# Optimization experiments

Measured on AMD Instinct MI355X. Metric: run time of the kernel, lower is better.

Reference implementation:

```python
import jax, jax.numpy as jnp
import numpy as np

B, N, F = 64, 512, 128

def setup_inputs() -> dict:
    key = jax.random.key(0)
    k1, k2 = jax.random.split(key)
    inp = jax.random.normal(k1, (B, N, F), dtype=jnp.float32)
    valid_mask = jnp.ones((B, N, N), dtype=jnp.float32)
    weight = 0.1 * jax.random.normal(k2, (N, N), dtype=jnp.float32)
    return {"input": inp, "valid_mask": valid_mask, "weight": weight}

def reference(input, valid_mask, weight):
    # softmax over last dim of weight, broadcast over batch
    adj = jax.nn.softmax(weight, axis=-1)[None, :, :] * valid_mask  # [B,N,N]
    n = weight.shape[0]
    adj = adj + jnp.eye(n, dtype=adj.dtype)[None, :, :]
    # symmetric degree normalization D^-1/2 A D^-1/2 (D diagonal of row sums).
    # Original builds dense D and does two matmuls; diagonal scaling is the
    # identical math expressed as row/col broadcast.
    row_sum = adj.sum(axis=2)  # [B,N]
    d = jnp.where(row_sum > 0, jax.lax.rsqrt(row_sum), 0.0)  # inf -> 0 handling
    adj_nor = d[:, :, None] * adj * d[:, None, :]  # [B,N,N]
    return jnp.matmul(adj_nor, input)  # [B,N,F]
```

## Files before the change

kernel.cpp:

```cpp
#include <hip/hip_runtime.h>
#include <math.h>

#define BB 64
#define NN 512
#define FF 128

typedef __bf16 bf16x8 __attribute__((ext_vector_type(8)));
typedef float floatx4 __attribute__((ext_vector_type(4)));

__device__ __forceinline__ unsigned int bf16u(float f) {
    unsigned int u = __builtin_bit_cast(unsigned int, f);
    unsigned int r = (u + 0x7FFFu + ((u >> 16) & 1u)) >> 16;
    return r & 0xFFFFu;
}

__global__ __launch_bounds__(256) void softmax_kernel(const float* __restrict__ w,
                                                      float* __restrict__ S) {
    const int row = blockIdx.x;
    const float* wr = w + (size_t)row * NN;
    float* sr = S + (size_t)row * NN;
    const int tid = threadIdx.x;
    const int wave = tid >> 6, lane = tid & 63;

    float v0 = wr[tid];
    float v1 = wr[tid + 256];

    float m = fmaxf(v0, v1);
    #pragma unroll
    for (int off = 32; off > 0; off >>= 1)
        m = fmaxf(m, __shfl_down(m, off, 64));
    __shared__ float red[8];
    if (lane == 0) red[wave] = m;
    __syncthreads();
    if (tid == 0) red[4] = fmaxf(fmaxf(red[0], red[1]), fmaxf(red[2], red[3]));
    __syncthreads();
    m = red[4];

    float e0 = expf(v0 - m);
    float e1 = expf(v1 - m);

    float s = e0 + e1;
    #pragma unroll
    for (int off = 32; off > 0; off >>= 1)
        s += __shfl_down(s, off, 64);
    __syncthreads();
    if (lane == 0) red[wave] = s;
    __syncthreads();
    if (tid == 0) red[5] = 1.0f / (red[0] + red[1] + red[2] + red[3]);
    __syncthreads();
    const float inv = red[5];

    sr[tid]       = e0 * inv;
    sr[tid + 256] = e1 * inv;
}

__global__ __launch_bounds__(256) void rowsum_kernel(const float* __restrict__ S,
                                                     const float* __restrict__ mask,
                                                     float* __restrict__ dvec) {
    const int b = blockIdx.x >> 5;
    const int g = blockIdx.x & 31;
    const int r = threadIdx.x >> 4;
    const int l = threadIdx.x & 15;
    const int i = g * 16 + r;

    const float4* mrow = (const float4*)(mask + ((size_t)b * NN + i) * NN);
    const float4* srow = (const float4*)(S + (size_t)i * NN);

    float sum = 0.f;
    #pragma unroll
    for (int k = 0; k < 8; ++k) {
        float4 mv = mrow[l + 16 * k];
        float4 sv = srow[l + 16 * k];
        sum += mv.x * sv.x + mv.y * sv.y + mv.z * sv.z + mv.w * sv.w;
    }
    #pragma unroll
    for (int off = 8; off > 0; off >>= 1)
        sum += __shfl_down(sum, off, 16);
    if (l == 0) {
        float rs = sum + 1.0f;
        dvec[b * NN + i] = (rs > 0.f) ? (1.0f / sqrtf(rs)) : 0.f;
    }
}

#define PADT 129
__global__ __launch_bounds__(256) void xt_kernel(const float* __restrict__ in,
                                                 const float* __restrict__ dvec,
                                                 unsigned short* __restrict__ Xt) {
    __shared__ unsigned short T[64 * PADT];
    const int b = blockIdx.y;
    const int j0 = blockIdx.x * 64;
    const int tid = threadIdx.x;

    const int fg = tid & 31;
    const int jr = tid >> 5;
    #pragma unroll
    for (int p = 0; p < 8; ++p) {
        int j = jr + 8 * p;
        float dj = dvec[b * NN + j0 + j];
        float4 xv = *(const float4*)(in + ((size_t)b * NN + j0 + j) * FF + 4 * fg);
        T[j * PADT + 4 * fg + 0] = (unsigned short)bf16u(xv.x * dj);
        T[j * PADT + 4 * fg + 1] = (unsigned short)bf16u(xv.y * dj);
        T[j * PADT + 4 * fg + 2] = (unsigned short)bf16u(xv.z * dj);
        T[j * PADT + 4 * fg + 3] = (unsigned short)bf16u(xv.w * dj);
    }
    __syncthreads();

    const int c = tid & 7;
    const int fr = tid >> 3;
    #pragma unroll
    for (int q = 0; q < 4; ++q) {
        int f = fr + 32 * q;
        unsigned int v01 = (unsigned int)T[(8 * c + 0) * PADT + f] |
                           ((unsigned int)T[(8 * c + 1) * PADT + f] << 16);
        unsigned int v23 = (unsigned int)T[(8 * c + 2) * PADT + f] |
                           ((unsigned int)T[(8 * c + 3) * PADT + f] << 16);
        unsigned int v45 = (unsigned int)T[(8 * c + 4) * PADT + f] |
                           ((unsigned int)T[(8 * c + 5) * PADT + f] << 16);
        unsigned int v67 = (unsigned int)T[(8 * c + 6) * PADT + f] |
                           ((unsigned int)T[(8 * c + 7) * PADT + f] << 16);
        uint4 pk = make_uint4(v01, v23, v45, v67);
        *(uint4*)(Xt + ((size_t)b * FF + f) * NN + j0 + 8 * c) = pk;
    }
}

#define TI 32
#define ASTR 72
__global__ __launch_bounds__(256) void matmul_kernel(const float* __restrict__ S,
                                                     const float* __restrict__ mask,
                                                     const float* __restrict__ dvec,
                                                     const unsigned short* __restrict__ Xt,
                                                     const float* __restrict__ in,
                                                     float* __restrict__ out) {
    __shared__ __align__(16) unsigned short Alds[2][TI * ASTR];

    const int b = blockIdx.y;
    const int i_base = blockIdx.x * TI;
    const int tid = threadIdx.x;
    const int w = tid >> 6;
    const int lane = tid & 63;
    const int quad = lane >> 4;
    const int l16 = lane & 15;
    const int iw = (w & 1) * 16;
    const int fw = (w >> 1) * 64;

    const float* dB = dvec + b * NN;
    const unsigned short* XtB = Xt + (size_t)b * FF * NN;

    floatx4 acc[4];
    #pragma unroll
    for (int nt = 0; nt < 4; nt++) acc[nt] = (floatx4){0.f, 0.f, 0.f, 0.f};

    const int a_il = tid >> 3;
    const int a_js = (tid & 7) * 8;
    const float* mbase = mask + ((size_t)b * NN + i_base + a_il) * NN + a_js;
    const float* sbase = S + (size_t)(i_base + a_il) * NN + a_js;
    unsigned short* awr = &Alds[0][0] + a_il * ASTR + a_js;

    {
        float4 m0 = *(const float4*)(mbase);
        float4 m1 = *(const float4*)(mbase + 4);
        float4 s0 = *(const float4*)(sbase);
        float4 s1 = *(const float4*)(sbase + 4);
        uint4 pk;
        pk.x = bf16u(m0.x * s0.x) | (bf16u(m0.y * s0.y) << 16);
        pk.y = bf16u(m0.z * s0.z) | (bf16u(m0.w * s0.w) << 16);
        pk.z = bf16u(m1.x * s1.x) | (bf16u(m1.y * s1.y) << 16);
        pk.w = bf16u(m1.z * s1.z) | (bf16u(m1.w * s1.w) << 16);
        *(uint4*)awr = pk;
    }

    #pragma unroll
    for (int c = 0; c < 8; ++c) {
        const int p = c & 1;
        float4 m0, m1, s0, s1;
        if (c < 7) {
            int jn = (c + 1) * 64;
            m0 = *(const float4*)(mbase + jn);
            m1 = *(const float4*)(mbase + jn + 4);
            s0 = *(const float4*)(sbase + jn);
            s1 = *(const float4*)(sbase + jn + 4);
        }
        __syncthreads();

        const int j0 = c * 64;
        bf16x8 bfr[2][4];
        #pragma unroll
        for (int s = 0; s < 2; ++s)
            #pragma unroll
            for (int nt = 0; nt < 4; ++nt)
                bfr[s][nt] = *(const bf16x8*)&XtB[(size_t)(fw + nt * 16 + l16) * NN + j0 + s * 32 + quad * 8];
        #pragma unroll
        for (int s = 0; s < 2; ++s) {
            bf16x8 af = *(const bf16x8*)&Alds[p][(iw + l16) * ASTR + s * 32 + quad * 8];
            #pragma unroll
            for (int nt = 0; nt < 4; ++nt)
                acc[nt] = __builtin_amdgcn_mfma_f32_16x16x32_bf16(af, bfr[s][nt], acc[nt], 0, 0, 0);
        }

        if (c < 7) {
            uint4 pk;
            pk.x = bf16u(m0.x * s0.x) | (bf16u(m0.y * s0.y) << 16);
            pk.y = bf16u(m0.z * s0.z) | (bf16u(m0.w * s0.w) << 16);
            pk.z = bf16u(m1.x * s1.x) | (bf16u(m1.y * s1.y) << 16);
            pk.w = bf16u(m1.z * s1.z) | (bf16u(m1.w * s1.w) << 16);
            *(uint4*)(&Alds[p ^ 1][0] + a_il * ASTR + a_js) = pk;
        }
    }

    #pragma unroll
    for (int nt = 0; nt < 4; nt++) {
        int f = fw + nt * 16 + l16;
        #pragma unroll
        for (int r = 0; r < 4; r++) {
            int i = i_base + iw + quad * 4 + r;
            float di = dB[i];
            float x = in[((size_t)b * NN + i) * FF + f];
            out[((size_t)b * NN + i) * FF + f] = di * (acc[nt][r] + di * x);
        }
    }
}

extern "C" void kernel_launch(void* const* d_in, const int* in_sizes, int n_in,
                              void* d_out, int out_size, void* d_ws, size_t ws_size,
                              hipStream_t stream) {
    const float* inp  = (const float*)d_in[0];
    const float* mask = (const float*)d_in[1];
    const float* w    = (const float*)d_in[2];
    float* out = (float*)d_out;

    unsigned short* Xt = (unsigned short*)d_ws;
    float* S    = (float*)(Xt + (size_t)BB * FF * NN);
    float* dvec = S + (size_t)NN * NN;

    softmax_kernel<<<NN, 256, 0, stream>>>(w, S);
    rowsum_kernel<<<BB * 32, 256, 0, stream>>>(S, mask, dvec);
    dim3 gx(NN / 64, BB);
    xt_kernel<<<gx, 256, 0, stream>>>(inp, dvec, Xt);
    dim3 g3(NN / TI, BB);
    matmul_kernel<<<g3, 256, 0, stream>>>(S, mask, dvec, Xt, inp, out);
}
```

Baseline: 154.2 us.

## Fuse softmax with rowsum, shrink matmul row tile, prefetch B fragments

Merges the softmax and the masked row-sum/rsqrt into one kernel. Each block recomputes the softmax row and handles 16 batches for that row, which removes one launch and the global reread of S for the row sums. The matmul tile shrinks from 32 to 16 rows, doubling the block count to 2048 for better occupancy. Each wave now covers 32 features, so X fragments are reloaded by more blocks and reuse drops. The Xt fragments are also register-prefetched one chunk ahead to hide global load latency.

```diff
diff --git a/kernel.cpp b/kernel.cpp
--- a/kernel.cpp
+++ b/kernel.cpp
@@ -4,6 +4,9 @@
 #define BB 64
 #define NN 512
 #define FF 128
+#define ASTR 72
+#define PADT 129
+#define TI2 16
 
 typedef __bf16 bf16x8 __attribute__((ext_vector_type(8)));
 typedef float floatx4 __attribute__((ext_vector_type(4)));
@@ -14,23 +17,24 @@
     return r & 0xFFFFu;
 }
 
-__global__ __launch_bounds__(256) void softmax_kernel(const float* __restrict__ w,
-                                                      float* __restrict__ S) {
+__global__ __launch_bounds__(256) void softmax_rowsum_kernel(
+        const float* __restrict__ w, const float* __restrict__ mask,
+        float* __restrict__ S, float* __restrict__ dvec) {
+    __shared__ float Srow[NN];
+    __shared__ float red[8];
     const int row = blockIdx.x;
-    const float* wr = w + (size_t)row * NN;
-    float* sr = S + (size_t)row * NN;
+    const int bg = blockIdx.y;
     const int tid = threadIdx.x;
-    const int wave = tid >> 6, lane = tid & 63;
-
-    float v0 = wr[tid];
-    float v1 = wr[tid + 256];
+    const int wv = tid >> 6, lane = tid & 63;
+
+    float v0 = w[(size_t)row * NN + tid];
+    float v1 = w[(size_t)row * NN + tid + 256];
 
     float m = fmaxf(v0, v1);
     #pragma unroll
     for (int off = 32; off > 0; off >>= 1)
         m = fmaxf(m, __shfl_down(m, off, 64));
-    __shared__ float red[8];
-    if (lane == 0) red[wave] = m;
+    if (lane == 0) red[wv] = m;
     __syncthreads();
     if (tid == 0) red[4] = fmaxf(fmaxf(red[0], red[1]), fmaxf(red[2], red[3]));
     __syncthreads();
@@ -38,51 +42,52 @@
 
     float e0 = expf(v0 - m);
     float e1 = expf(v1 - m);
-
     float s = e0 + e1;
     #pragma unroll
     for (int off = 32; off > 0; off >>= 1)
         s += __shfl_down(s, off, 64);
     __syncthreads();
-    if (lane == 0) red[wave] = s;
+    if (lane == 0) red[wv] = s;
     __syncthreads();
     if (tid == 0) red[5] = 1.0f / (red[0] + red[1] + red[2] + red[3]);
     __syncthreads();
     const float inv = red[5];
-
-    sr[tid]       = e0 * inv;
-    sr[tid + 256] = e1 * inv;
-}
-
-__global__ __launch_bounds__(256) void rowsum_kernel(const float* __restrict__ S,
-                                                     const float* __restrict__ mask,
-                                                     float* __restrict__ dvec) {
-    const int b = blockIdx.x >> 5;
-    const int g = blockIdx.x & 31;
-    const int r = threadIdx.x >> 4;
-    const int l = threadIdx.x & 15;
-    const int i = g * 16 + r;
-
-    const float4* mrow = (const float4*)(mask + ((size_t)b * NN + i) * NN);
-    const float4* srow = (const float4*)(S + (size_t)i * NN);
-
-    float sum = 0.f;
-    #pragma unroll
-    for (int k = 0; k < 8; ++k) {
-        float4 mv = mrow[l + 16 * k];
-        float4 sv = srow[l + 16 * k];
-        sum += mv.x * sv.x + mv.y * sv.y + mv.z * sv.z + mv.w * sv.w;
-    }
-    #pragma unroll
-    for (int off = 8; off > 0; off >>= 1)
-        sum += __shfl_down(sum, off, 16);
-    if (l == 0) {
-        float rs = sum + 1.0f;
-        dvec[b * NN + i] = (rs > 0.f) ? (1.0f / sqrtf(rs)) : 0.f;
-    }
-}
-
-#define PADT 129
+    const float s0v = e0 * inv, s1v = e1 * inv;
+
+    Srow[tid] = s0v;
+    Srow[tid + 256] = s1v;
+    if (bg == 0) {
+        S[(size_t)row * NN + tid] = s0v;
+        S[(size_t)row * NN + tid + 256] = s1v;
+    }
+    __syncthreads();
+
+    float4 sA = *(const float4*)&Srow[lane * 8];
+    float4 sB = *(const float4*)&Srow[lane * 8 + 4];
+
+    float4 mA[4], mB[4];
+    #pragma unroll
+    for (int t = 0; t < 4; ++t) {
+        int b = bg * 16 + wv * 4 + t;
+        const float4* mrow = (const float4*)(mask + ((size_t)b * NN + row) * NN);
+        mA[t] = mrow[2 * lane];
+        mB[t] = mrow[2 * lane + 1];
+    }
+    #pragma unroll
+    for (int t = 0; t < 4; ++t) {
+        float sum = mA[t].x * sA.x + mA[t].y * sA.y + mA[t].z * sA.z + mA[t].w * sA.w
+                  + mB[t].x * sB.x + mB[t].y * sB.y + mB[t].z * sB.z + mB[t].w * sB.w;
+        #pragma unroll
+        for (int off = 32; off > 0; off >>= 1)
+            sum += __shfl_down(sum, off, 64);
+        if (lane == 0) {
+            int b = bg * 16 + wv * 4 + t;
+            float rs = sum + 1.0f;
+            dvec[b * NN + row] = (rs > 0.f) ? (1.0f / sqrtf(rs)) : 0.f;
+        }
+    }
+}
+
 __global__ __launch_bounds__(256) void xt_kernel(const float* __restrict__ in,
                                                  const float* __restrict__ dvec,
                                                  unsigned short* __restrict__ Xt) {
@@ -104,7 +109,6 @@
         T[j * PADT + 4 * fg + 3] = (unsigned short)bf16u(xv.w * dj);
     }
     __syncthreads();
-
     const int c = tid & 7;
     const int fr = tid >> 3;
     #pragma unroll
@@ -118,101 +122,96 @@
                            ((unsigned int)T[(8 * c + 5) * PADT + f] << 16);
         unsigned int v67 = (unsigned int)T[(8 * c + 6) * PADT + f] |
                            ((unsigned int)T[(8 * c + 7) * PADT + f] << 16);
-        uint4 pk = make_uint4(v01, v23, v45, v67);
-        *(uint4*)(Xt + ((size_t)b * FF + f) * NN + j0 + 8 * c) = pk;
-    }
-}
-
-#define TI 32
-#define ASTR 72
-__global__ __launch_bounds__(256) void matmul_kernel(const float* __restrict__ S,
-                                                     const float* __restrict__ mask,
-                                                     const float* __restrict__ dvec,
-                                                     const unsigned short* __restrict__ Xt,
-                                                     const float* __restrict__ in,
-                                                     float* __restrict__ out) {
-    __shared__ __align__(16) unsigned short Alds[2][TI * ASTR];
+        *(uint4*)(Xt + ((size_t)b * FF + f) * NN + j0 + 8 * c) = make_uint4(v01, v23, v45, v67);
+    }
+}
+
+__global__ __launch_bounds__(256) void matmul_kernel(
+        const float* __restrict__ S, const float* __restrict__ mask,
+        const float* __restrict__ dvec, const unsigned short* __restrict__ Xt,
+        const float* __restrict__ in, float* __restrict__ out) {
+    __shared__ __align__(16) unsigned short Alds[2][TI2 * ASTR];
 
     const int b = blockIdx.y;
-    const int i_base = blockIdx.x * TI;
+    const int i_base = blockIdx.x * TI2;
     const int tid = threadIdx.x;
-    const int w = tid >> 6;
+    const int wv = tid >> 6;
     const int lane = tid & 63;
     const int quad = lane >> 4;
     const int l16 = lane & 15;
-    const int iw = (w & 1) * 16;
-    const int fw = (w >> 1) * 64;
+    const int fw = wv * 32;
 
     const float* dB = dvec + b * NN;
     const unsigned short* XtB = Xt + (size_t)b * FF * NN;
 
-    floatx4 acc[4];
-    #pragma unroll
-    for (int nt = 0; nt < 4; nt++) acc[nt] = (floatx4){0.f, 0.f, 0.f, 0.f};
-
-    const int a_il = tid >> 3;
-    const int a_js = (tid & 7) * 8;
+    floatx4 acc[2];
+    acc[0] = (floatx4){0.f, 0.f, 0.f, 0.f};
+    acc[1] = (floatx4){0.f, 0.f, 0.f, 0.f};
+
+    const int a_il = tid >> 4;
+    const int a_js = (tid & 15) * 4;
     const float* mbase = mask + ((size_t)b * NN + i_base + a_il) * NN + a_js;
     const float* sbase = S + (size_t)(i_base + a_il) * NN + a_js;
-    unsigned short* awr = &Alds[0][0] + a_il * ASTR + a_js;
 
     {
-        float4 m0 = *(const float4*)(mbase);
-        float4 m1 = *(const float4*)(mbase + 4);
-        float4 s0 = *(const float4*)(sbase);
-        float4 s1 = *(const float4*)(sbase + 4);
-        uint4 pk;
+        float4 m0 = *(const float4*)mbase;
+        float4 s0 = *(const float4*)sbase;
+        uint2 pk;
         pk.x = bf16u(m0.x * s0.x) | (bf16u(m0.y * s0.y) << 16);
         pk.y = bf16u(m0.z * s0.z) | (bf16u(m0.w * s0.w) << 16);
-        pk.z = bf16u(m1.x * s1.x) | (bf16u(m1.y * s1.y) << 16);
-        pk.w = bf16u(m1.z * s1.z) | (bf16u(m1.w * s1.w) << 16);
-        *(uint4*)awr = pk;
-    }
+        *(uint2*)(&Alds[0][0] + a_il * ASTR + a_js) = pk;
+    }
+    bf16x8 bcur[4];
+    #pragma unroll
+    for (int s = 0; s < 2; ++s)
+        #pragma unroll
+        for (int nt = 0; nt < 2; ++nt)
+            bcur[s * 2 + nt] = *(const bf16x8*)&XtB[(size_t)(fw + nt * 16 + l16) * NN + s * 32 + quad * 8];
 
     #pragma unroll
     for (int c = 0; c < 8; ++c) {
         const int p = c & 1;
-        float4 m0, m1, s0, s1;
+        float4 m0, s0;
+        if (c < 7) {
+            m0 = *(const float4*)(mbase + (c + 1) * 64);
+            s0 = *(const float4*)(sbase + (c + 1) * 64);
+        }
+        __syncthreads();
+
+        bf16x8 bnxt[4];
         if (c < 7) {
             int jn = (c + 1) * 64;
-            m0 = *(const float4*)(mbase + jn);
-            m1 = *(const float4*)(mbase + jn + 4);
-            s0 = *(const float4*)(sbase + jn);
-            s1 = *(const float4*)(sbase + jn + 4);
-        }
-        __syncthreads();
-
-        const int j0 = c * 64;
-        bf16x8 bfr[2][4];
-        #pragma unroll
-        for (int s = 0; s < 2; ++s)
             #pragma unroll
-            for (int nt = 0; nt < 4; ++nt)
-                bfr[s][nt] = *(const bf16x8*)&XtB[(size_t)(fw + nt * 16 + l16) * NN + j0 + s * 32 + quad * 8];
+            for (int s = 0; s < 2; ++s)
+                #pragma unroll
+                for (int nt = 0; nt < 2; ++nt)
+                    bnxt[s * 2 + nt] = *(const bf16x8*)&XtB[(size_t)(fw + nt * 16 + l16) * NN + jn + s * 32 + quad * 8];
+        }
+
         #pragma unroll
         for (int s = 0; s < 2; ++s) {
-            bf16x8 af = *(const bf16x8*)&Alds[p][(iw + l16) * ASTR + s * 32 + quad * 8];
+            bf16x8 af = *(const bf16x8*)&Alds[p][l16 * ASTR + s * 32 + quad * 8];
             #pragma unroll
-            for (int nt = 0; nt < 4; ++nt)
-                acc[nt] = __builtin_amdgcn_mfma_f32_16x16x32_bf16(af, bfr[s][nt], acc[nt], 0, 0, 0);
+            for (int nt = 0; nt < 2; ++nt)
+                acc[nt] = __builtin_amdgcn_mfma_f32_16x16x32_bf16(af, bcur[s * 2 + nt], acc[nt], 0, 0, 0);
         }
 
         if (c < 7) {
-            uint4 pk;
+            uint2 pk;
             pk.x = bf16u(m0.x * s0.x) | (bf16u(m0.y * s0.y) << 16);
             pk.y = bf16u(m0.z * s0.z) | (bf16u(m0.w * s0.w) << 16);
-            pk.z = bf16u(m1.x * s1.x) | (bf16u(m1.y * s1.y) << 16);
-            pk.w = bf16u(m1.z * s1.z) | (bf16u(m1.w * s1.w) << 16);
-            *(uint4*)(&Alds[p ^ 1][0] + a_il * ASTR + a_js) = pk;
-        }
-    }
-
-    #pragma unroll
-    for (int nt = 0; nt < 4; nt++) {
+            *(uint2*)(&Alds[p ^ 1][0] + a_il * ASTR + a_js) = pk;
+            #pragma unroll
+            for (int q = 0; q < 4; ++q) bcur[q] = bnxt[q];
+        }
+    }
+
+    #pragma unroll
+    for (int nt = 0; nt < 2; ++nt) {
         int f = fw + nt * 16 + l16;
         #pragma unroll
-        for (int r = 0; r < 4; r++) {
-            int i = i_base + iw + quad * 4 + r;
+        for (int r = 0; r < 4; ++r) {
+            int i = i_base + quad * 4 + r;
             float di = dB[i];
             float x = in[((size_t)b * NN + i) * FF + f];
             out[((size_t)b * NN + i) * FF + f] = di * (acc[nt][r] + di * x);
@@ -232,10 +231,7 @@
     float* S    = (float*)(Xt + (size_t)BB * FF * NN);
     float* dvec = S + (size_t)NN * NN;
 
-    softmax_kernel<<<NN, 256, 0, stream>>>(w, S);
-    rowsum_kernel<<<BB * 32, 256, 0, stream>>>(S, mask, dvec);
-    dim3 gx(NN / 64, BB);
-    xt_kernel<<<gx, 256, 0, stream>>>(inp, dvec, Xt);
-    dim3 g3(NN / TI, BB);
-    matmul_kernel<<<g3, 256, 0, stream>>>(S, mask, dvec, Xt, inp, out);
-}
+    softmax_rowsum_kernel<<<dim3(NN, 4), 256, 0, stream>>>(w, mask, S, dvec);
+    xt_kernel<<<dim3(NN / 64, BB), 256, 0, stream>>>(inp, dvec, Xt);
+    matmul_kernel<<<dim3(NN / TI2, BB), 256, 0, stream>>>(S, mask, dvec, Xt, inp, out);
+}
```

Measured after the change: 147.3 us. 4.5% less time.
